# Kernel optimization log

Hardware: AMD Instinct MI355X
Metric: run time of the kernel (lower is better)

The kernel has to match this reference:

```python
import jax, jax.numpy as jnp
import numpy as np

N, K = 4096, 32          # batch, max active features per position
D = 49152                # half_feature_numel
BASE = 512               # base_dim
F0, F1 = 768, 64         # inter_dims of the two factored blocks


def setup_inputs() -> dict:
    key = jax.random.key(0)
    ks = jax.random.split(key, 8)
    return {
        "x_val": jnp.ones((N, K), dtype=jnp.float32),
        "W_aff": jax.random.normal(ks[0], (BASE, D), dtype=jnp.float32) * 0.01,
        "b_aff": jax.random.normal(ks[1], (BASE,), dtype=jnp.float32) * 0.01,
        "w_block0": jax.random.normal(ks[2], (F0, BASE), dtype=jnp.float32) * 0.01,
        "w_block1": jax.random.normal(ks[3], (F1, BASE), dtype=jnp.float32) * 0.01,
        "x_idx": jax.random.randint(ks[4], (N, K), 0, D, dtype=jnp.int32),
        "f0": jax.random.randint(ks[5], (D,), 0, F0, dtype=jnp.int32),
        "f1": jax.random.randint(ks[6], (D,), 0, F1, dtype=jnp.int32),
    }


def reference(x_val, W_aff, b_aff, w_block0, w_block1, x_idx, f0, f1):
    # affine(x): for sparse x, x_dense @ W_aff.T + b == sum_k v[n,k] * W_aff[:, idx[n,k]] + b
    aff_cols = W_aff.T[x_idx]                       # [N, K, BASE] gathered columns
    out = jnp.einsum('nk,nkd->nd', x_val, aff_cols) + b_aff
    # FactoredBlock: remap active indices through f, densify (duplicates sum), matmul.
    # Equivalent gather form: sum_k v[n,k] * weights[f[idx[n,k]]]
    out = out + jnp.einsum('nk,nkd->nd', x_val, w_block0[f0[x_idx]])
    out = out + jnp.einsum('nk,nkd->nd', x_val, w_block1[f1[x_idx]])
    return out
```

## Files before the change

### kernel.cpp

```cpp
#include <hip/hip_runtime.h>

#define N_BATCH 4096
#define K_ACT   32
#define D_FEAT  49152
#define BASE    512

typedef unsigned short ushort_t;
typedef __attribute__((ext_vector_type(8))) unsigned short ushort8;

__device__ __forceinline__ ushort_t f2bf(float f) {
    unsigned u = __builtin_bit_cast(unsigned, f);
    u += 0x7FFFu + ((u >> 16) & 1u);
    return (ushort_t)(u >> 16);
}

__global__ __launch_bounds__(1024) void build_R_kernel(
    const float* __restrict__ W_aff,
    const float* __restrict__ w0,
    const float* __restrict__ w1,
    const int* __restrict__ f0,
    const int* __restrict__ f1,
    ushort_t* __restrict__ Rb)
{
    __shared__ float tile[128 * 128];
    const int r0 = blockIdx.x * 128;
    const int d0 = blockIdx.y * 128;
    const int t  = threadIdx.x;

    {
        const int x   = t & 31;
        const int rl0 = t >> 5;
        const float4* W4 = (const float4*)W_aff;
#pragma unroll
        for (int i = 0; i < 4; ++i) {
            const int rl = rl0 + 32 * i;
            float4 w = W4[(size_t)(r0 + rl) * (D_FEAT / 4) + (d0 >> 2) + x];
            const int S = (rl & 31) ^ (rl >> 5);
            ((float4*)tile)[rl * 32 + (x ^ S)] = w;
        }
    }
    __syncthreads();

    const int dl  = t & 127;
    const int seg = t >> 7;
    const int d   = d0 + dl;
    const int g   = dl >> 2;
    const int e   = dl & 3;

    float a[16];
#pragma unroll
    for (int j = 0; j < 16; ++j) {
        const int rl = seg * 16 + j;
        const int S  = (rl & 31) ^ (rl >> 5);
        a[j] = tile[rl * 128 + ((g ^ S) << 2) + e];
    }

    const int i0 = f0[d];
    const int i1 = f1[d];
    const float4* w0v = (const float4*)w0;
    const float4* w1v = (const float4*)w1;
    const size_t b0base = (size_t)i0 * (BASE / 4) + (r0 >> 2) + seg * 4;
    const size_t b1base = (size_t)i1 * (BASE / 4) + (r0 >> 2) + seg * 4;
#pragma unroll
    for (int q = 0; q < 4; ++q) {
        const float4 b0 = w0v[b0base + q];
        const float4 b1 = w1v[b1base + q];
        a[4 * q + 0] += b0.x + b1.x;
        a[4 * q + 1] += b0.y + b1.y;
        a[4 * q + 2] += b0.z + b1.z;
        a[4 * q + 3] += b0.w + b1.w;
    }

    ushort_t* dst = &Rb[(size_t)d * BASE + r0 + seg * 16];
#pragma unroll
    for (int q = 0; q < 2; ++q) {
        ushort8 o;
#pragma unroll
        for (int j = 0; j < 8; ++j) o[j] = f2bf(a[8 * q + j]);
        *(ushort8*)&dst[8 * q] = o;
    }
}

__global__ __launch_bounds__(256) void gather_out_kernel(
    const ushort_t* __restrict__ Rb,
    const float* __restrict__ x_val,
    const int*   __restrict__ x_idx,
    const float* __restrict__ b_aff,
    float* __restrict__ out)
{
    const int lane = threadIdx.x & 63;
    const int wv   = threadIdx.x >> 6;
    const int n    = blockIdx.x * 4 + wv;

    float acc[8];
    {
        const float4 bb0 = ((const float4*)b_aff)[2 * lane];
        const float4 bb1 = ((const float4*)b_aff)[2 * lane + 1];
        acc[0] = bb0.x; acc[1] = bb0.y; acc[2] = bb0.z; acc[3] = bb0.w;
        acc[4] = bb1.x; acc[5] = bb1.y; acc[6] = bb1.z; acc[7] = bb1.w;
    }

    const int*   idxp = x_idx + (size_t)n * K_ACT;
    const float* valp = x_val + (size_t)n * K_ACT;

#pragma unroll
    for (int k = 0; k < K_ACT; ++k) {
        const int   idx = idxp[k];
        const float v   = valp[k];
        const ushort8 w = *(const ushort8*)&Rb[(size_t)idx * BASE + 8 * lane];
#pragma unroll
        for (int j = 0; j < 8; ++j) {
            const float wf = __builtin_bit_cast(float, (unsigned)w[j] << 16);
            acc[j] = fmaf(v, wf, acc[j]);
        }
    }

    float4 o0, o1;
    o0.x = acc[0]; o0.y = acc[1]; o0.z = acc[2]; o0.w = acc[3];
    o1.x = acc[4]; o1.y = acc[5]; o1.z = acc[6]; o1.w = acc[7];
    ((float4*)out)[(size_t)n * (BASE / 4) + 2 * lane]     = o0;
    ((float4*)out)[(size_t)n * (BASE / 4) + 2 * lane + 1] = o1;
}

__global__ __launch_bounds__(512) void direct_kernel(
    const float* __restrict__ x_val,
    const float* __restrict__ W_aff,
    const float* __restrict__ b_aff,
    const float* __restrict__ w0,
    const float* __restrict__ w1,
    const int*   __restrict__ x_idx,
    const int*   __restrict__ f0,
    const int*   __restrict__ f1,
    float* __restrict__ out)
{
    const int n = blockIdx.x;
    const int r = threadIdx.x;
    float acc = b_aff[r];
    for (int k = 0; k < K_ACT; ++k) {
        const int   idx = x_idx[(size_t)n * K_ACT + k];
        const float v   = x_val[(size_t)n * K_ACT + k];
        float w = W_aff[(size_t)r * D_FEAT + idx];
        w += w0[(size_t)f0[idx] * BASE + r];
        w += w1[(size_t)f1[idx] * BASE + r];
        acc += v * w;
    }
    out[(size_t)n * BASE + r] = acc;
}

extern "C" void kernel_launch(void* const* d_in, const int* in_sizes, int n_in,
                              void* d_out, int out_size, void* d_ws, size_t ws_size,
                              hipStream_t stream) {
    const float* x_val = (const float*)d_in[0];
    const float* W_aff = (const float*)d_in[1];
    const float* b_aff = (const float*)d_in[2];
    const float* w0    = (const float*)d_in[3];
    const float* w1    = (const float*)d_in[4];
    const int*   x_idx = (const int*)d_in[5];
    const int*   f0    = (const int*)d_in[6];
    const int*   f1    = (const int*)d_in[7];
    float* out = (float*)d_out;

    const size_t needR = (size_t)D_FEAT * BASE * sizeof(ushort_t);
    if (ws_size >= needR) {
        ushort_t* Rb = (ushort_t*)d_ws;
        dim3 grid(BASE / 128, D_FEAT / 128);
        build_R_kernel<<<grid, 1024, 0, stream>>>(W_aff, w0, w1, f0, f1, Rb);
        gather_out_kernel<<<N_BATCH / 4, 256, 0, stream>>>(Rb, x_val, x_idx, b_aff, out);
    } else {
        direct_kernel<<<N_BATCH, BASE, 0, stream>>>(x_val, W_aff, b_aff, w0, w1,
                                                    x_idx, f0, f1, out);
    }
}
```

Measured before the change: 217.6 us.

## Store precomputed bf16 table as four 128-column panels instead of row-major

Changes the layout of the precomputed combined weight table Rb from [D][512] row-major to four panels of [D][128]. The build kernel writes each block's 128-column slice into its own panel, with each quarter-wavefront writing one contiguous 256-byte row. The gather kernel maps each 16-lane group of a wave to one panel, so a wave touches four separate 256-byte segments per index instead of one 1 KB row. The goal is coalesced writes in the build phase, at the cost of more scattered reads during the gather.

```diff
diff --git a/kernel.cpp b/kernel.cpp
--- a/kernel.cpp
+++ b/kernel.cpp
@@ -4,6 +4,8 @@
 #define K_ACT   32
 #define D_FEAT  49152
 #define BASE    512
+#define PANEL_R 128
+#define PANEL_ELEMS ((size_t)D_FEAT * PANEL_R)
 
 typedef unsigned short ushort_t;
 typedef __attribute__((ext_vector_type(8))) unsigned short ushort8;
@@ -23,7 +25,8 @@
     ushort_t* __restrict__ Rb)
 {
     __shared__ float tile[128 * 128];
-    const int r0 = blockIdx.x * 128;
+    const int p  = blockIdx.x;
+    const int r0 = p * 128;
     const int d0 = blockIdx.y * 128;
     const int t  = threadIdx.x;
 
@@ -41,43 +44,45 @@
     }
     __syncthreads();
 
-    const int dl  = t & 127;
-    const int seg = t >> 7;
-    const int d   = d0 + dl;
-    const int g   = dl >> 2;
-    const int e   = dl & 3;
-
-    float a[16];
-#pragma unroll
-    for (int j = 0; j < 16; ++j) {
-        const int rl = seg * 16 + j;
-        const int S  = (rl & 31) ^ (rl >> 5);
-        a[j] = tile[rl * 128 + ((g ^ S) << 2) + e];
-    }
-
-    const int i0 = f0[d];
-    const int i1 = f1[d];
+    const int w_  = t >> 6;
+    const int l   = t & 63;
+    const int lg  = l >> 4;
+    const int lr  = l & 15;
     const float4* w0v = (const float4*)w0;
     const float4* w1v = (const float4*)w1;
-    const size_t b0base = (size_t)i0 * (BASE / 4) + (r0 >> 2) + seg * 4;
-    const size_t b1base = (size_t)i1 * (BASE / 4) + (r0 >> 2) + seg * 4;
+    ushort_t* panel = Rb + (size_t)p * PANEL_ELEMS;
+
 #pragma unroll
-    for (int q = 0; q < 4; ++q) {
-        const float4 b0 = w0v[b0base + q];
-        const float4 b1 = w1v[b1base + q];
-        a[4 * q + 0] += b0.x + b1.x;
-        a[4 * q + 1] += b0.y + b1.y;
-        a[4 * q + 2] += b0.z + b1.z;
-        a[4 * q + 3] += b0.w + b1.w;
-    }
+    for (int s = 0; s < 2; ++s) {
+        const int dl = w_ * 8 + s * 4 + lg;
+        const int d  = d0 + dl;
+        const int g  = dl >> 2;
+        const int e  = dl & 3;
 
-    ushort_t* dst = &Rb[(size_t)d * BASE + r0 + seg * 16];
+        float a[8];
 #pragma unroll
-    for (int q = 0; q < 2; ++q) {
+        for (int j = 0; j < 8; ++j) {
+            const int rl = lr * 8 + j;
+            const int S  = (rl & 31) ^ (rl >> 5);
+            a[j] = tile[rl * 128 + ((g ^ S) << 2) + e];
+        }
+
+        const int i0 = f0[d];
+        const int i1 = f1[d];
+        const size_t bb = (size_t)(r0 >> 2) + lr * 2;
+        const float4 b0 = w0v[(size_t)i0 * (BASE / 4) + bb];
+        const float4 b1 = w0v[(size_t)i0 * (BASE / 4) + bb + 1];
+        const float4 c0 = w1v[(size_t)i1 * (BASE / 4) + bb];
+        const float4 c1 = w1v[(size_t)i1 * (BASE / 4) + bb + 1];
+        a[0] += b0.x + c0.x;  a[1] += b0.y + c0.y;
+        a[2] += b0.z + c0.z;  a[3] += b0.w + c0.w;
+        a[4] += b1.x + c1.x;  a[5] += b1.y + c1.y;
+        a[6] += b1.z + c1.z;  a[7] += b1.w + c1.w;
+
         ushort8 o;
 #pragma unroll
-        for (int j = 0; j < 8; ++j) o[j] = f2bf(a[8 * q + j]);
-        *(ushort8*)&dst[8 * q] = o;
+        for (int j = 0; j < 8; ++j) o[j] = f2bf(a[j]);
+        *(ushort8*)&panel[(size_t)d * PANEL_R + lr * 8] = o;
     }
 }
 
@@ -91,11 +96,16 @@
     const int lane = threadIdx.x & 63;
     const int wv   = threadIdx.x >> 6;
     const int n    = blockIdx.x * 4 + wv;
+    const int p    = lane >> 4;
+    const int lr   = lane & 15;
+
+    const ushort_t* prow = Rb + (size_t)p * PANEL_ELEMS + lr * 8;
+    const int fo = p * 32 + lr * 2;
 
     float acc[8];
     {
-        const float4 bb0 = ((const float4*)b_aff)[2 * lane];
-        const float4 bb1 = ((const float4*)b_aff)[2 * lane + 1];
+        const float4 bb0 = ((const float4*)b_aff)[fo];
+        const float4 bb1 = ((const float4*)b_aff)[fo + 1];
         acc[0] = bb0.x; acc[1] = bb0.y; acc[2] = bb0.z; acc[3] = bb0.w;
         acc[4] = bb1.x; acc[5] = bb1.y; acc[6] = bb1.z; acc[7] = bb1.w;
     }
@@ -107,7 +117,7 @@
     for (int k = 0; k < K_ACT; ++k) {
         const int   idx = idxp[k];
         const float v   = valp[k];
-        const ushort8 w = *(const ushort8*)&Rb[(size_t)idx * BASE + 8 * lane];
+        const ushort8 w = *(const ushort8*)&prow[(size_t)idx * PANEL_R];
 #pragma unroll
         for (int j = 0; j < 8; ++j) {
             const float wf = __builtin_bit_cast(float, (unsigned)w[j] << 16);
@@ -118,8 +128,8 @@
     float4 o0, o1;
     o0.x = acc[0]; o0.y = acc[1]; o0.z = acc[2]; o0.w = acc[3];
     o1.x = acc[4]; o1.y = acc[5]; o1.z = acc[6]; o1.w = acc[7];
-    ((float4*)out)[(size_t)n * (BASE / 4) + 2 * lane]     = o0;
-    ((float4*)out)[(size_t)n * (BASE / 4) + 2 * lane + 1] = o1;
+    ((float4*)out)[(size_t)n * (BASE / 4) + fo]     = o0;
+    ((float4*)out)[(size_t)n * (BASE / 4) + fo + 1] = o1;
 }
 
 __global__ __launch_bounds__(512) void direct_kernel(
```

Result: faster. 199.1 us (-8.5%).
